# Optimization experiments

Hardware: AMD Instinct MI355X
Metric: run time of the kernel (lower is better)

## Reference

```python
import jax, jax.numpy as jnp
import numpy as np

N_NODES = 50000
N_EDGES = 800000
D = 64  # in_dim = hidden = out_dim
LEAKY_SLOPE = 0.01  # F.leaky_relu default


def gat_layer(h, src, dst, W, b, aW, ab):
    # fc: z = h @ W.T + b            [N, D_out]
    z = h @ W.T + b
    zs = z[src]                       # gather src feats  [E, D_out]
    zd = z[dst]                       # gather dst feats  [E, D_out]
    # attn_fc(concat(z_src, z_dst)) -> scalar per edge, then leaky_relu
    e = jnp.concatenate([zs, zd], axis=-1) @ aW.T + ab   # [E, 1]
    e = jax.nn.leaky_relu(e, LEAKY_SLOPE)[:, 0]          # [E]
    # softmax over incoming edges per destination node (mailbox softmax)
    m = jax.ops.segment_max(e, dst, num_segments=N_NODES)    # [N]
    ex = jnp.exp(e - m[dst])
    den = jax.ops.segment_sum(ex, dst, num_segments=N_NODES)  # [N]
    alpha = ex / den[dst]                                      # [E]
    # scatter-sum aggregate of alpha * z_src
    return jax.ops.segment_sum(alpha[:, None] * zs, dst, num_segments=N_NODES)


def setup_inputs() -> dict:
    key = jax.random.key(0)
    ks = jax.random.split(key, 16)
    x = jax.random.normal(ks[0], (N_NODES, D), dtype=jnp.float32)
    src = jax.random.randint(ks[1], (N_EDGES,), 0, N_NODES)
    dst = jax.random.randint(ks[2], (N_EDGES,), 0, N_NODES)
    # xavier_normal with relu gain, per reset_parameters
    gain = float(np.sqrt(2.0))
    params = {}
    for i in range(3):
        std_fc = gain * np.sqrt(2.0 / (D + D))
        std_at = gain * np.sqrt(2.0 / (2 * D + 1))
        params[f"W{i}"] = jax.random.normal(ks[3 + 4 * i], (D, D), dtype=jnp.float32) * std_fc
        params[f"b{i}"] = jnp.zeros((D,), dtype=jnp.float32)
        params[f"a{i}"] = jax.random.normal(ks[4 + 4 * i], (1, 2 * D), dtype=jnp.float32) * std_at
        params[f"ab{i}"] = jnp.zeros((1,), dtype=jnp.float32)
    return {"x": x, "src": src, "dst": dst, **params}


def reference(x, src, dst, W0, b0, a0, ab0, W1, b1, a1, ab1, W2, b2, a2, ab2):
    h = gat_layer(x, src, dst, W0, b0, a0, ab0)
    h = jax.nn.relu(h)
    h = gat_layer(h, src, dst, W1, b1, a1, ab1)
    h = jax.nn.relu(h)
    h = gat_layer(h, src, dst, W2, b2, a2, ab2)
    return h
```

## Files before the change

### kernel.cpp

```cpp
#include <hip/hip_runtime.h>
#include <math.h>

#define N_NODES 50000
#define N_EDGES 800000
#define D 64

#define NB 256
#define NBLK 256
#define BUCKET_NODES 196
#define TILE 3125

typedef unsigned short ushort_t;

__device__ __forceinline__ ushort_t f32_to_bf16(float f) {
    unsigned u = __float_as_uint(f);
    u += 0x7fffu + ((u >> 16) & 1u);
    return (ushort_t)(u >> 16);
}

template<int N>
__global__ void scan_partial_g(const int* __restrict__ in, int* __restrict__ partials) {
    const int base = blockIdx.x * 1024 + threadIdx.x * 4;
    int4 c = make_int4(0, 0, 0, 0);
    if (base + 3 < N) c = *(const int4*)&in[base];
    else { int* cp = (int*)&c; for (int j = 0; j < 4; ++j) if (base + j < N) cp[j] = in[base + j]; }
    int s = c.x + c.y + c.z + c.w;
    #pragma unroll
    for (int off = 32; off >= 1; off >>= 1) s += __shfl_xor(s, off, 64);
    __shared__ int red[4];
    if ((threadIdx.x & 63) == 0) red[threadIdx.x >> 6] = s;
    __syncthreads();
    if (threadIdx.x == 0) partials[blockIdx.x] = red[0] + red[1] + red[2] + red[3];
}

template<int N, int NT>
__global__ void scan_write_i(const int* __restrict__ in, const int* __restrict__ partials_raw,
                             int* __restrict__ out) {
    __shared__ int toff;
    __shared__ int sh[256];
    const int tid = threadIdx.x;
    if (tid < 64) {
        const int v = (tid < NT) ? partials_raw[tid] : 0;
        int inc = v;
        #pragma unroll
        for (int off = 1; off < 64; off <<= 1) {
            const int w = __shfl_up(inc, off, 64);
            if (tid >= off) inc += w;
        }
        if (tid == blockIdx.x) toff = inc - v;
    }
    const int base = blockIdx.x * 1024 + tid * 4;
    int4 c = make_int4(0, 0, 0, 0);
    if (base + 3 < N) c = *(const int4*)&in[base];
    else { int* cp = (int*)&c; for (int j = 0; j < 4; ++j) if (base + j < N) cp[j] = in[base + j]; }
    const int s = c.x + c.y + c.z + c.w;
    sh[tid] = s;
    __syncthreads();
    for (int off = 1; off < 256; off <<= 1) {
        const int w = (tid >= off) ? sh[tid - off] : 0;
        __syncthreads();
        sh[tid] += w;
        __syncthreads();
    }
    int run = toff + sh[tid] - s;
    const int* cp = (const int*)&c;
    int rp[4];
    #pragma unroll
    for (int j = 0; j < 4; ++j) { rp[j] = run; run += cp[j]; }
    if (base + 3 < N) *(int4*)&out[base] = make_int4(rp[0], rp[1], rp[2], rp[3]);
    else for (int j = 0; j < 4; ++j) if (base + j < N) out[base + j] = rp[j];
}

__global__ __launch_bounds__(256) void bucket_hist(const int* __restrict__ dst,
                                                   int* __restrict__ Acnt) {
    __shared__ int hist[NB];
    for (int i = threadIdx.x; i < NB; i += 256) hist[i] = 0;
    __syncthreads();
    const int base = blockIdx.x * TILE;
    for (int i = threadIdx.x; i < TILE; i += 256)
        atomicAdd(&hist[dst[base + i] / BUCKET_NODES], 1);
    __syncthreads();
    for (int bk = threadIdx.x; bk < NB; bk += 256)
        Acnt[bk * NBLK + blockIdx.x] = hist[bk];
}

__global__ __launch_bounds__(256) void bucket_scatter(const int* __restrict__ src,
                                                      const int* __restrict__ dst,
                                                      const int* __restrict__ offs,
                                                      int2* __restrict__ staging) {
    __shared__ int cur[NB];
    for (int i = threadIdx.x; i < NB; i += 256) cur[i] = offs[i * NBLK + blockIdx.x];
    __syncthreads();
    const int base = blockIdx.x * TILE;
    for (int i = threadIdx.x; i < TILE; i += 256) {
        const int s = src[base + i], d = dst[base + i];
        const int pos = atomicAdd(&cur[d / BUCKET_NODES], 1);
        staging[pos] = make_int2(s, d);
    }
}

__global__ __launch_bounds__(256) void node_counts(const int2* __restrict__ staging,
                                                   const int* __restrict__ offs,
                                                   int* __restrict__ counts,
                                                   int* __restrict__ bucket_sum) {
    __shared__ int cnt[BUCKET_NODES];
    __shared__ int red[4];
    const int b = blockIdx.x, tid = threadIdx.x;
    for (int i = tid; i < BUCKET_NODES; i += 256) cnt[i] = 0;
    __syncthreads();
    const int s0 = offs[b * NBLK];
    const int s1 = (b == NB - 1) ? N_EDGES : offs[(b + 1) * NBLK];
    for (int i = s0 + tid; i < s1; i += 256)
        atomicAdd(&cnt[staging[i].y - b * BUCKET_NODES], 1);
    __syncthreads();
    for (int i = tid; i < BUCKET_NODES; i += 256) {
        const int node = b * BUCKET_NODES + i;
        if (node < N_NODES) counts[node] = cnt[i];
    }
    int s = (tid < BUCKET_NODES) ? cnt[tid] : 0;
    #pragma unroll
    for (int off = 32; off >= 1; off >>= 1) s += __shfl_xor(s, off, 64);
    if ((tid & 63) == 0) red[tid >> 6] = s;
    __syncthreads();
    if (tid == 0) bucket_sum[b] = red[0] + red[1] + red[2] + red[3];
}

__global__ __launch_bounds__(256) void row_ptr_build(const int* __restrict__ counts,
                                                     const int* __restrict__ bucket_sum,
                                                     int* __restrict__ row_ptr) {
    __shared__ int bs[NB];
    __shared__ int loc[256];
    const int b = blockIdx.x, tid = threadIdx.x;
    bs[tid] = bucket_sum[tid];
    __syncthreads();
    for (int off = 1; off < 256; off <<= 1) {
        const int w = (tid >= off) ? bs[tid - off] : 0;
        __syncthreads();
        bs[tid] += w;
        __syncthreads();
    }
    const int bucket_off = bs[b] - bucket_sum[b];
    const int node = b * BUCKET_NODES + tid;
    const int c = (tid < BUCKET_NODES && node < N_NODES) ? counts[node] : 0;
    loc[tid] = c;
    __syncthreads();
    for (int off = 1; off < 256; off <<= 1) {
        const int w = (tid >= off) ? loc[tid - off] : 0;
        __syncthreads();
        loc[tid] += w;
        __syncthreads();
    }
    if (tid < BUCKET_NODES && node < N_NODES) row_ptr[node] = bucket_off + loc[tid] - c;
    if (b == 0 && tid == 0) row_ptr[N_NODES] = N_EDGES;
}

__global__ __launch_bounds__(256) void bucket_to_csr(const int2* __restrict__ staging,
                                                     const int* __restrict__ offs,
                                                     const int* __restrict__ row_ptr,
                                                     int* __restrict__ csr_src) {
    __shared__ int cur[BUCKET_NODES];
    const int b = blockIdx.x;
    for (int i = threadIdx.x; i < BUCKET_NODES; i += 256) {
        const int node = b * BUCKET_NODES + i;
        cur[i] = (node < N_NODES) ? row_ptr[node] : 0;
    }
    __syncthreads();
    const int s0 = offs[b * NBLK];
    const int s1 = (b == NB - 1) ? N_EDGES : offs[(b + 1) * NBLK];
    for (int i = s0 + threadIdx.x; i < s1; i += 256) {
        const int2 e = staging[i];
        const int pos = atomicAdd(&cur[e.y - b * BUCKET_NODES], 1);
        csr_src[pos] = e.x;
    }
}

#define NL_ROWS 8
__global__ __launch_bounds__(256) void node_linear_gemm(
    const float* __restrict__ h, ushort_t* __restrict__ zb,
    const float* __restrict__ W, const float* __restrict__ b,
    const float* __restrict__ a, const float* __restrict__ ab,
    float* __restrict__ s_src, float* __restrict__ s_dst)
{
    __shared__ float Wt[64 * 65];
    for (int idx = threadIdx.x; idx < D * D; idx += 256) {
        const int j = idx >> 6, k = idx & 63;
        Wt[k * 65 + j] = W[idx];
    }
    __syncthreads();

    const int lane = threadIdx.x & 63;
    const int wv   = __builtin_amdgcn_readfirstlane(threadIdx.x >> 6);
    const int row0 = (blockIdx.x * 4 + wv) * NL_ROWS;
    if (row0 >= N_NODES) return;

    const float bj  = b[lane];
    const float alo = a[lane];
    const float ahi = a[64 + lane];

    const float* hr[NL_ROWS];
    #pragma unroll
    for (int r = 0; r < NL_ROWS; ++r) hr[r] = h + (size_t)(row0 + r) * D;

    float acc[NL_ROWS];
    #pragma unroll
    for (int r = 0; r < NL_ROWS; ++r) acc[r] = bj;

    #pragma unroll 4
    for (int k = 0; k < D; ++k) {
        const float wkj = Wt[k * 65 + lane];
        #pragma unroll
        for (int r = 0; r < NL_ROWS; ++r)
            acc[r] = fmaf(hr[r][k], wkj, acc[r]);
    }

    #pragma unroll
    for (int r = 0; r < NL_ROWS; ++r) {
        zb[(size_t)(row0 + r) * D + lane] = f32_to_bf16(acc[r]);
        float u = acc[r] * alo;
        float v = acc[r] * ahi;
        #pragma unroll
        for (int off = 32; off >= 1; off >>= 1) {
            u += __shfl_xor(u, off, 64);
            v += __shfl_xor(v, off, 64);
        }
        if (lane == 0) { s_src[row0 + r] = u; s_dst[row0 + r] = v + ab[0]; }
    }
}

template<bool RELU>
__global__ __launch_bounds__(256) void fused_softmax_gather(
    const int* __restrict__ row_ptr, const int* __restrict__ csr_src,
    const float* __restrict__ s_src, const float* __restrict__ s_dst,
    const ushort_t* __restrict__ zb, float* __restrict__ out)
{
    __shared__ int2 sh[4][4][64];
    const int lane = threadIdx.x & 63;
    const int wv   = threadIdx.x >> 6;
    const int g    = lane >> 4;
    const int sl   = lane & 15;
    const int node0 = (blockIdx.x * 4 + wv) * 4;
    if (node0 >= N_NODES) return;
    const int mynode = node0 + g;

    const int beg = row_ptr[mynode];
    const int end = row_ptr[mynode + 1];
    const float sd = s_dst[mynode];
    float m = -INFINITY, den = 0.f;
    for (int base = beg; base < end; base += 16) {
        const int n = min(16, end - base);
        float e = -INFINITY;
        if (sl < n) {
            const int s = csr_src[base + sl];
            e = s_src[s] + sd;
            e = e > 0.f ? e : 0.01f * e;
        }
        float mc = e;
        #pragma unroll
        for (int off = 8; off >= 1; off >>= 1) mc = fmaxf(mc, __shfl_xor(mc, off, 64));
        if (mc > m) { den *= __expf(m - mc); m = mc; }
        float ex = (sl < n) ? __expf(e - m) : 0.f;
        #pragma unroll
        for (int off = 8; off >= 1; off >>= 1) ex += __shfl_xor(ex, off, 64);
        den += ex;
    }
    const float invden = (den > 0.f) ? 1.f / den : 0.f;

    int begq[4], endq[4];
    float mq[4], ivq[4], sdq[4];
    #pragma unroll
    for (int q = 0; q < 4; ++q) {
        begq[q] = __shfl(beg, q * 16, 64);
        endq[q] = __shfl(end, q * 16, 64);
        mq[q]   = __shfl(m, q * 16, 64);
        ivq[q]  = __shfl(invden, q * 16, 64);
        sdq[q]  = __shfl(sd, q * 16, 64);
    }
    int maxdeg = 0;
    #pragma unroll
    for (int q = 0; q < 4; ++q) maxdeg = max(maxdeg, endq[q] - begq[q]);

    const int half = lane >> 5;
    const int fl   = lane & 31;
    float2 acc[4][2];
    #pragma unroll
    for (int q = 0; q < 4; ++q) {
        acc[q][0] = make_float2(0.f, 0.f);
        acc[q][1] = make_float2(0.f, 0.f);
    }

    for (int c = 0; c < maxdeg; c += 64) {
        #pragma unroll
        for (int q = 0; q < 4; ++q) {
            int2 ws = make_int2(0, 0);
            const int i = begq[q] + c + lane;
            if (i < endq[q]) {
                const int s = csr_src[i];
                float e = s_src[s] + sdq[q];
                e = e > 0.f ? e : 0.01f * e;
                ws = make_int2(__float_as_int(__expf(e - mq[q]) * ivq[q]), s);
            }
            sh[wv][q][lane] = ws;
        }
        const int n = min(64, maxdeg - c);
        for (int t = 0; t < n; t += 4) {
            #pragma unroll
            for (int q = 0; q < 4; ++q) {
                const int2 wa = sh[wv][q][t + half];
                const int2 wb = sh[wv][q][t + 2 + half];
                const unsigned ua = *(const unsigned*)&zb[(size_t)wa.y * D + 2 * fl];
                const unsigned ub = *(const unsigned*)&zb[(size_t)wb.y * D + 2 * fl];
                const float fa = __int_as_float(wa.x);
                const float fb = __int_as_float(wb.x);
                acc[q][0].x = fmaf(fa, __uint_as_float(ua << 16), acc[q][0].x);
                acc[q][0].y = fmaf(fa, __uint_as_float(ua & 0xffff0000u), acc[q][0].y);
                acc[q][1].x = fmaf(fb, __uint_as_float(ub << 16), acc[q][1].x);
                acc[q][1].y = fmaf(fb, __uint_as_float(ub & 0xffff0000u), acc[q][1].y);
            }
        }
    }
    #pragma unroll
    for (int q = 0; q < 4; ++q) {
        float2 tot = make_float2(acc[q][0].x + acc[q][1].x,
                                 acc[q][0].y + acc[q][1].y);
        tot.x += __shfl_xor(tot.x, 32, 64);
        tot.y += __shfl_xor(tot.y, 32, 64);
        if (RELU) { tot.x = fmaxf(tot.x, 0.f); tot.y = fmaxf(tot.y, 0.f); }
        if (half == 0)
            *(float2*)&out[(size_t)(node0 + q) * D + 2 * fl] = tot;
    }
}

extern "C" void kernel_launch(void* const* d_in, const int* in_sizes, int n_in,
                              void* d_out, int out_size, void* d_ws, size_t ws_size,
                              hipStream_t stream) {
    const float* x   = (const float*)d_in[0];
    const int*   src = (const int*)d_in[1];
    const int*   dst = (const int*)d_in[2];
    float* out = (float*)d_out;

    char* wp = (char*)d_ws;
    auto alloc = [&](size_t bytes) -> void* {
        void* p = (void*)wp;
        wp += (bytes + 255) & ~(size_t)255;
        return p;
    };
    ushort_t* zb      = (ushort_t*)alloc((size_t)N_NODES * D * sizeof(ushort_t));
    float* s_src      = (float*)alloc((size_t)N_NODES * sizeof(float));
    float* s_dst      = (float*)alloc((size_t)N_NODES * sizeof(float));
    int*   counts     = (int*)alloc((size_t)N_NODES * sizeof(int));
    int*   row_ptr    = (int*)alloc((size_t)(N_NODES + 1) * sizeof(int));
    int*   csr_src    = (int*)alloc((size_t)N_EDGES * sizeof(int));
    int*   partB      = (int*)alloc(64 * sizeof(int));
    int*   bucket_sum = (int*)alloc((size_t)NB * sizeof(int));
    int*   Acnt       = (int*)alloc((size_t)NB * NBLK * sizeof(int));
    int*   offs       = (int*)alloc((size_t)NB * NBLK * sizeof(int));
    int2*  staging    = (int2*)alloc((size_t)N_EDGES * sizeof(int2));
    (void)ws_size;

    bucket_hist<<<NBLK, 256, 0, stream>>>(dst, Acnt);
    scan_partial_g<NB * NBLK><<<64, 256, 0, stream>>>(Acnt, partB);
    scan_write_i<NB * NBLK, 64><<<64, 256, 0, stream>>>(Acnt, partB, offs);
    bucket_scatter<<<NBLK, 256, 0, stream>>>(src, dst, offs, staging);
    node_counts<<<NB, 256, 0, stream>>>(staging, offs, counts, bucket_sum);
    row_ptr_build<<<NB, 256, 0, stream>>>(counts, bucket_sum, row_ptr);
    bucket_to_csr<<<NB, 256, 0, stream>>>(staging, offs, row_ptr, csr_src);

    const int grid_k1 = (N_NODES + 4 * NL_ROWS - 1) / (4 * NL_ROWS);
    const int grid_fg = N_NODES / 16;

    for (int layer = 0; layer < 3; ++layer) {
        const float* W  = (const float*)d_in[3 + 4 * layer];
        const float* b  = (const float*)d_in[4 + 4 * layer];
        const float* a  = (const float*)d_in[5 + 4 * layer];
        const float* ab = (const float*)d_in[6 + 4 * layer];
        const float* hin = (layer == 0) ? x : out;

        node_linear_gemm<<<grid_k1, 256, 0, stream>>>(hin, zb, W, b, a, ab, s_src, s_dst);
        if (layer < 2) {
            fused_softmax_gather<true ><<<grid_fg, 256, 0, stream>>>(row_ptr, csr_src, s_src, s_dst, zb, out);
        } else {
            fused_softmax_gather<false><<<grid_fg, 256, 0, stream>>>(row_ptr, csr_src, s_src, s_dst, zb, out);
        }
    }
}
```

Measured before the change: 197.5 us.

## Replace per-node softmax max pass with global upper-bound shift and deferred normalization

The GEMM kernel now also computes a global maximum of s_src per layer, using an atomicMax on an order-preserving unsigned key. The gather kernel uses leaky_relu(gmax + s_dst) as a per-node upper bound on the logits instead of the exact segment max. This removes the separate max/denominator pass over each node's edges. The denominator is accumulated during the single weight pass and applied at the end. The risk is underflow in exp when a node's logits sit far below the bound, which can lose precision or collapse the denominator to zero.

New measurement: 370.2 us. 1.87x slower.

```diff
diff --git a/kernel.cpp b/kernel.cpp
--- a/kernel.cpp
+++ b/kernel.cpp
@@ -16,6 +16,14 @@
     unsigned u = __float_as_uint(f);
     u += 0x7fffu + ((u >> 16) & 1u);
     return (ushort_t)(u >> 16);
+}
+__device__ __forceinline__ unsigned fkey(float f) {
+    unsigned b = __float_as_uint(f);
+    return (b & 0x80000000u) ? ~b : (b | 0x80000000u);
+}
+__device__ __forceinline__ float funkey(unsigned u) {
+    unsigned b = (u & 0x80000000u) ? (u ^ 0x80000000u) : ~u;
+    return __uint_as_float(b);
 }
 
 template<int N>
@@ -179,7 +187,8 @@
     const float* __restrict__ h, ushort_t* __restrict__ zb,
     const float* __restrict__ W, const float* __restrict__ b,
     const float* __restrict__ a, const float* __restrict__ ab,
-    float* __restrict__ s_src, float* __restrict__ s_dst)
+    float* __restrict__ s_src, float* __restrict__ s_dst,
+    unsigned* __restrict__ gmax_u)
 {
     __shared__ float Wt[64 * 65];
     for (int idx = threadIdx.x; idx < D * D; idx += 256) {
@@ -213,6 +222,7 @@
             acc[r] = fmaf(hr[r][k], wkj, acc[r]);
     }
 
+    float umax = -INFINITY;
     #pragma unroll
     for (int r = 0; r < NL_ROWS; ++r) {
         zb[(size_t)(row0 + r) * D + lane] = f32_to_bf16(acc[r]);
@@ -223,69 +233,48 @@
             u += __shfl_xor(u, off, 64);
             v += __shfl_xor(v, off, 64);
         }
+        umax = fmaxf(umax, u);
         if (lane == 0) { s_src[row0 + r] = u; s_dst[row0 + r] = v + ab[0]; }
     }
+    if (lane == 0) atomicMax(gmax_u, fkey(umax));
 }
 
 template<bool RELU>
-__global__ __launch_bounds__(256) void fused_softmax_gather(
+__global__ __launch_bounds__(256) void fused_gather_ub(
     const int* __restrict__ row_ptr, const int* __restrict__ csr_src,
     const float* __restrict__ s_src, const float* __restrict__ s_dst,
+    const unsigned* __restrict__ gmax_u,
     const ushort_t* __restrict__ zb, float* __restrict__ out)
 {
     __shared__ int2 sh[4][4][64];
     const int lane = threadIdx.x & 63;
-    const int wv   = threadIdx.x >> 6;
-    const int g    = lane >> 4;
-    const int sl   = lane & 15;
+    const int wv   = __builtin_amdgcn_readfirstlane(threadIdx.x >> 6);
     const int node0 = (blockIdx.x * 4 + wv) * 4;
     if (node0 >= N_NODES) return;
-    const int mynode = node0 + g;
-
-    const int beg = row_ptr[mynode];
-    const int end = row_ptr[mynode + 1];
-    const float sd = s_dst[mynode];
-    float m = -INFINITY, den = 0.f;
-    for (int base = beg; base < end; base += 16) {
-        const int n = min(16, end - base);
-        float e = -INFINITY;
-        if (sl < n) {
-            const int s = csr_src[base + sl];
-            e = s_src[s] + sd;
-            e = e > 0.f ? e : 0.01f * e;
-        }
-        float mc = e;
-        #pragma unroll
-        for (int off = 8; off >= 1; off >>= 1) mc = fmaxf(mc, __shfl_xor(mc, off, 64));
-        if (mc > m) { den *= __expf(m - mc); m = mc; }
-        float ex = (sl < n) ? __expf(e - m) : 0.f;
-        #pragma unroll
-        for (int off = 8; off >= 1; off >>= 1) ex += __shfl_xor(ex, off, 64);
-        den += ex;
-    }
-    const float invden = (den > 0.f) ? 1.f / den : 0.f;
+    const float gmax = funkey(*gmax_u);
 
     int begq[4], endq[4];
-    float mq[4], ivq[4], sdq[4];
+    float sdq[4], mubq[4];
+    int maxdeg = 0;
     #pragma unroll
     for (int q = 0; q < 4; ++q) {
-        begq[q] = __shfl(beg, q * 16, 64);
-        endq[q] = __shfl(end, q * 16, 64);
-        mq[q]   = __shfl(m, q * 16, 64);
-        ivq[q]  = __shfl(invden, q * 16, 64);
-        sdq[q]  = __shfl(sd, q * 16, 64);
-    }
-    int maxdeg = 0;
-    #pragma unroll
-    for (int q = 0; q < 4; ++q) maxdeg = max(maxdeg, endq[q] - begq[q]);
+        begq[q] = row_ptr[node0 + q];
+        endq[q] = row_ptr[node0 + q + 1];
+        sdq[q]  = s_dst[node0 + q];
+        const float mu = gmax + sdq[q];
+        mubq[q] = mu > 0.f ? mu : 0.01f * mu;
+        maxdeg = max(maxdeg, endq[q] - begq[q]);
+    }
 
     const int half = lane >> 5;
     const int fl   = lane & 31;
     float2 acc[4][2];
+    float denl[4];
     #pragma unroll
     for (int q = 0; q < 4; ++q) {
         acc[q][0] = make_float2(0.f, 0.f);
         acc[q][1] = make_float2(0.f, 0.f);
+        denl[q] = 0.f;
     }
 
     for (int c = 0; c < maxdeg; c += 64) {
@@ -297,7 +286,9 @@
                 const int s = csr_src[i];
                 float e = s_src[s] + sdq[q];
                 e = e > 0.f ? e : 0.01f * e;
-                ws = make_int2(__float_as_int(__expf(e - mq[q]) * ivq[q]), s);
+                const float w = __expf(e - mubq[q]);
+                denl[q] += w;
+                ws = make_int2(__float_as_int(w), s);
             }
             sh[wv][q][lane] = ws;
         }
@@ -320,13 +311,18 @@
     }
     #pragma unroll
     for (int q = 0; q < 4; ++q) {
+        float den = denl[q];
+        #pragma unroll
+        for (int off = 32; off >= 1; off >>= 1) den += __shfl_xor(den, off, 64);
         float2 tot = make_float2(acc[q][0].x + acc[q][1].x,
                                  acc[q][0].y + acc[q][1].y);
         tot.x += __shfl_xor(tot.x, 32, 64);
         tot.y += __shfl_xor(tot.y, 32, 64);
-        if (RELU) { tot.x = fmaxf(tot.x, 0.f); tot.y = fmaxf(tot.y, 0.f); }
+        const float inv = (den > 0.f) ? 1.f / den : 0.f;
+        float2 v = make_float2(tot.x * inv, tot.y * inv);
+        if (RELU) { v.x = fmaxf(v.x, 0.f); v.y = fmaxf(v.y, 0.f); }
         if (half == 0)
-            *(float2*)&out[(size_t)(node0 + q) * D + 2 * fl] = tot;
+            *(float2*)&out[(size_t)(node0 + q) * D + 2 * fl] = v;
     }
 }
 
@@ -352,10 +348,13 @@
     int*   csr_src    = (int*)alloc((size_t)N_EDGES * sizeof(int));
     int*   partB      = (int*)alloc(64 * sizeof(int));
     int*   bucket_sum = (int*)alloc((size_t)NB * sizeof(int));
+    unsigned* gmax_u  = (unsigned*)alloc(4 * sizeof(unsigned));
     int*   Acnt       = (int*)alloc((size_t)NB * NBLK * sizeof(int));
     int*   offs       = (int*)alloc((size_t)NB * NBLK * sizeof(int));
     int2*  staging    = (int2*)alloc((size_t)N_EDGES * sizeof(int2));
     (void)ws_size;
+
+    hipMemsetAsync(gmax_u, 0, 4 * sizeof(unsigned), stream);
 
     bucket_hist<<<NBLK, 256, 0, stream>>>(dst, Acnt);
     scan_partial_g<NB * NBLK><<<64, 256, 0, stream>>>(Acnt, partB);
@@ -375,11 +374,14 @@
         const float* ab = (const float*)d_in[6 + 4 * layer];
         const float* hin = (layer == 0) ? x : out;
 
-        node_linear_gemm<<<grid_k1, 256, 0, stream>>>(hin, zb, W, b, a, ab, s_src, s_dst);
+        node_linear_gemm<<<grid_k1, 256, 0, stream>>>(hin, zb, W, b, a, ab,
+                                                      s_src, s_dst, &gmax_u[layer]);
         if (layer < 2) {
-            fused_softmax_gather<true ><<<grid_fg, 256, 0, stream>>>(row_ptr, csr_src, s_src, s_dst, zb, out);
+            fused_gather_ub<true ><<<grid_fg, 256, 0, stream>>>(row_ptr, csr_src, s_src, s_dst,
+                                                                &gmax_u[layer], zb, out);
         } else {
-            fused_softmax_gather<false><<<grid_fg, 256, 0, stream>>>(row_ptr, csr_src, s_src, s_dst, zb, out);
-        }
-    }
-}
+            fused_gather_ub<false><<<grid_fg, 256, 0, stream>>>(row_ptr, csr_src, s_src, s_dst,
+                                                                &gmax_u[layer], zb, out);
+        }
+    }
+}
```
